# Performance work log

Measured on AMD Instinct MI355X. Metric: run time of the kernel, lower is better.

The kernel has to match this reference:

```python
import jax, jax.numpy as jnp
import numpy as np


def _log_g(x):
    # log_g(x) = log(relu(x)+1) if x >= 0 else x
    return jnp.where(x >= 0, jnp.log1p(jnp.maximum(x, 0.0)), x)


def _min_gru(hg):
    # hg: [B, H, L] -> [B, H/2, L]
    h, gate = jnp.split(hg, 2, axis=1)
    log_coeffs = -jax.nn.softplus(gate)                    # log(1 - z)
    log_values = -jax.nn.softplus(-gate) + _log_g(h)       # log(z) + log g(h)
    a_star = jnp.cumsum(log_coeffs, axis=2)
    log_h0_plus_b_star = jax.lax.cumlogsumexp(log_values - a_star, axis=2)
    return jnp.exp(a_star + log_h0_plus_b_star)


def setup_inputs() -> dict:
    key = jax.random.key(0)
    B, H, L = 8, 512, 8192
    x = jax.random.normal(key, (B, H, L), dtype=jnp.float32)
    return {"x": x}


def reference(x) -> jnp.ndarray:
    # bidirectional minGRU: forward scan on first half of channels,
    # reversed scan on second half.
    fore, back = jnp.split(x, 2, axis=1)
    out_fore = _min_gru(fore)
    out_back = jnp.flip(_min_gru(jnp.flip(back, axis=2)), axis=2)
    return jnp.concatenate([out_fore, out_back], axis=1)  # [B, H/2, L]
```

## Files before the change

### kernel.cpp

```cpp
#include <hip/hip_runtime.h>
#include <math.h>


#define SEQ_L 8192
#define PER_LANE 8
#define SUB (64 * PER_LANE)
#define NSUB (SEQ_L / SUB)
#define DQ 4

__global__ __launch_bounds__(64, 2) void mingru_scan_kernel(
    const float* __restrict__ x, float* __restrict__ out) {
    const int blk = blockIdx.x;
    const int dir = blk >> 10;
    const int s   = blk & 1023;
    const int b   = s >> 7;
    const int c   = s & 127;
    const int lane = threadIdx.x;

    const float* __restrict__ hrow = x + (size_t)((b * 512) + (dir * 256) + c) * SEQ_L;
    const float* __restrict__ grow = hrow + (size_t)128 * SEQ_L;
    float* __restrict__ orow = out + (size_t)((b * 256) + (dir * 128) + c) * SEQ_L;

    float4 qh0[DQ], qh1[DQ], qg0[DQ], qg1[DQ];

#pragma unroll
    for (int k = 0; k < DQ; ++k) {
        const int base = k * SUB + lane * PER_LANE;
        const int p = dir ? (SEQ_L - base - PER_LANE) : base;
        qh0[k] = *(const float4*)(hrow + p);
        qh1[k] = *(const float4*)(hrow + p + 4);
        qg0[k] = *(const float4*)(grow + p);
        qg1[k] = *(const float4*)(grow + p + 4);
    }

    float carry = 0.0f;

#pragma unroll
    for (int t = 0; t < NSUB; ++t) {
        const int slot = t & (DQ - 1);
        const float4 h0 = qh0[slot], h1 = qh1[slot];
        const float4 g0 = qg0[slot], g1 = qg1[slot];

        if (t + DQ < NSUB) {
            const int nb = (t + DQ) * SUB + lane * PER_LANE;
            const int np = dir ? (SEQ_L - nb - PER_LANE) : nb;
            qh0[slot] = *(const float4*)(hrow + np);
            qh1[slot] = *(const float4*)(hrow + np + 4);
            qg0[slot] = *(const float4*)(grow + np);
            qg1[slot] = *(const float4*)(grow + np + 4);
        }

        float hv[PER_LANE], gv[PER_LANE];
        if (dir == 0) {
            hv[0]=h0.x; hv[1]=h0.y; hv[2]=h0.z; hv[3]=h0.w;
            hv[4]=h1.x; hv[5]=h1.y; hv[6]=h1.z; hv[7]=h1.w;
            gv[0]=g0.x; gv[1]=g0.y; gv[2]=g0.z; gv[3]=g0.w;
            gv[4]=g1.x; gv[5]=g1.y; gv[6]=g1.z; gv[7]=g1.w;
        } else {
            hv[0]=h1.w; hv[1]=h1.z; hv[2]=h1.y; hv[3]=h1.x;
            hv[4]=h0.w; hv[5]=h0.z; hv[6]=h0.y; hv[7]=h0.x;
            gv[0]=g1.w; gv[1]=g1.z; gv[2]=g1.y; gv[3]=g1.x;
            gv[4]=g0.w; gv[5]=g0.z; gv[6]=g0.y; gv[7]=g0.x;
        }

        float pp[PER_LANE], ov0[PER_LANE];
        float ca = 1.0f, cb = 0.0f;
#pragma unroll
        for (int j = 0; j < PER_LANE; ++j) {
            const float gt = gv[j];
            const float e  = __expf(-fabsf(gt));
            const float r  = 1.0f / (1.0f + e);
            const float sn = e * r;
            const float z  = (gt >= 0.0f) ? r  : sn;
            const float a  = (gt >= 0.0f) ? sn : r;
            const float hh = hv[j];
            const float gf = (hh >= 0.0f) ? (hh + 1.0f) : __expf(hh);
            const float bb = z * gf;
            cb = a * cb + bb;
            ca = a * ca;
            ov0[j] = cb;
            pp[j]  = ca;
        }

        float pa = ca, pb = cb;
#pragma unroll
        for (int d = 1; d < 64; d <<= 1) {
            const float oa = __shfl_up(pa, d);
            const float ob = __shfl_up(pb, d);
            if (lane >= d) {
                pb = pa * ob + pb;
                pa = pa * oa;
            }
        }

        float ea = __shfl_up(pa, 1);
        float eb = __shfl_up(pb, 1);
        if (lane == 0) { ea = 1.0f; eb = 0.0f; }
        const float st = ea * carry + eb;

        float ov[PER_LANE];
#pragma unroll
        for (int j = 0; j < PER_LANE; ++j) ov[j] = ov0[j] + st * pp[j];

        const int base = t * SUB + lane * PER_LANE;
        if (dir == 0) {
            *(float4*)(orow + base)     = make_float4(ov[0], ov[1], ov[2], ov[3]);
            *(float4*)(orow + base + 4) = make_float4(ov[4], ov[5], ov[6], ov[7]);
        } else {
            const int p = SEQ_L - base - PER_LANE;
            *(float4*)(orow + p)     = make_float4(ov[7], ov[6], ov[5], ov[4]);
            *(float4*)(orow + p + 4) = make_float4(ov[3], ov[2], ov[1], ov[0]);
        }

        const float ga = __shfl(pa, 63);
        const float gb = __shfl(pb, 63);
        carry = ga * carry + gb;
    }
}

extern "C" void kernel_launch(void* const* d_in, const int* in_sizes, int n_in,
                              void* d_out, int out_size, void* d_ws, size_t ws_size,
                              hipStream_t stream) {
    const float* x = (const float*)d_in[0];
    float* out = (float*)d_out;
    mingru_scan_kernel<<<2048, 64, 0, stream>>>(x, out);
}
```

Before: 218.3 us.

## Split sequential scan into chunk-aggregate, state-propagate, and apply kernels

Replaces the one-wavefront-per-sequence serial scan with a three-pass chunked scan. Pass one computes each 512-element chunk's affine aggregate, pass two serially propagates the carry across the 16 chunks of each sequence, and pass three recomputes the local scan with the carried-in state and writes the output. The goal is to expose far more parallelism than the original 2048 wavefronts with a 16-step serial dependency. The cost is reading the input twice, recomputing the gate math twice, and two extra kernel launches plus workspace traffic.

```diff
diff --git a/kernel.cpp b/kernel.cpp
--- a/kernel.cpp
+++ b/kernel.cpp
@@ -4,117 +4,149 @@
 
 #define SEQ_L 8192
 #define PER_LANE 8
-#define SUB (64 * PER_LANE)
-#define NSUB (SEQ_L / SUB)
-#define DQ 4
+#define CHUNK 512
+#define NCHUNK (SEQ_L / CHUNK)
+#define NSEQ 2048
+#define NCHUNK_TOTAL (NSEQ * NCHUNK)
 
-__global__ __launch_bounds__(64, 2) void mingru_scan_kernel(
-    const float* __restrict__ x, float* __restrict__ out) {
-    const int blk = blockIdx.x;
-    const int dir = blk >> 10;
-    const int s   = blk & 1023;
-    const int b   = s >> 7;
-    const int c   = s & 127;
-    const int lane = threadIdx.x;
+__device__ __forceinline__ void chunk_addr(const float* __restrict__ x,
+                                           int gchunk, int lane,
+                                           const float*& hrow, const float*& grow,
+                                           int& seq, int& k, int& dir, int& p) {
+    seq = gchunk >> 4;
+    k   = gchunk & 15;
+    dir = seq >> 10;
+    const int s = seq & 1023;
+    const int b = s >> 7;
+    const int c = s & 127;
+    hrow = x + (size_t)((b * 512) + (dir * 256) + c) * SEQ_L;
+    grow = hrow + (size_t)128 * SEQ_L;
+    const int base = k * CHUNK + lane * PER_LANE;
+    p = dir ? (SEQ_L - base - PER_LANE) : base;
+}
 
-    const float* __restrict__ hrow = x + (size_t)((b * 512) + (dir * 256) + c) * SEQ_L;
-    const float* __restrict__ grow = hrow + (size_t)128 * SEQ_L;
+__device__ __forceinline__ void load8(const float* hrow, const float* grow,
+                                      int p, int dir,
+                                      float* hv, float* gv) {
+    const float4 h0 = *(const float4*)(hrow + p);
+    const float4 h1 = *(const float4*)(hrow + p + 4);
+    const float4 g0 = *(const float4*)(grow + p);
+    const float4 g1 = *(const float4*)(grow + p + 4);
+    if (dir == 0) {
+        hv[0]=h0.x; hv[1]=h0.y; hv[2]=h0.z; hv[3]=h0.w;
+        hv[4]=h1.x; hv[5]=h1.y; hv[6]=h1.z; hv[7]=h1.w;
+        gv[0]=g0.x; gv[1]=g0.y; gv[2]=g0.z; gv[3]=g0.w;
+        gv[4]=g1.x; gv[5]=g1.y; gv[6]=g1.z; gv[7]=g1.w;
+    } else {
+        hv[0]=h1.w; hv[1]=h1.z; hv[2]=h1.y; hv[3]=h1.x;
+        hv[4]=h0.w; hv[5]=h0.z; hv[6]=h0.y; hv[7]=h0.x;
+        gv[0]=g1.w; gv[1]=g1.z; gv[2]=g1.y; gv[3]=g1.x;
+        gv[4]=g0.w; gv[5]=g0.z; gv[6]=g0.y; gv[7]=g0.x;
+    }
+}
+
+__device__ __forceinline__ void coeffs(float gt, float hh, float& a, float& bb) {
+    const float e  = __expf(-fabsf(gt));
+    const float r  = 1.0f / (1.0f + e);
+    const float sn = e * r;
+    const float z  = (gt >= 0.0f) ? r  : sn;
+    a  = (gt >= 0.0f) ? sn : r;
+    const float gf = (hh >= 0.0f) ? (hh + 1.0f) : __expf(hh);
+    bb = z * gf;
+}
+
+__global__ __launch_bounds__(256) void k_agg(const float* __restrict__ x,
+                                             float2* __restrict__ agg) {
+    const int lane = threadIdx.x & 63;
+    const int gchunk = blockIdx.x * 4 + (threadIdx.x >> 6);
+    const float *hrow, *grow; int seq, k, dir, p;
+    chunk_addr(x, gchunk, lane, hrow, grow, seq, k, dir, p);
+
+    float hv[PER_LANE], gv[PER_LANE];
+    load8(hrow, grow, p, dir, hv, gv);
+
+    float pa = 1.0f, pb = 0.0f;
+#pragma unroll
+    for (int j = 0; j < PER_LANE; ++j) {
+        float a, bb; coeffs(gv[j], hv[j], a, bb);
+        pb = a * pb + bb;
+        pa = a * pa;
+    }
+#pragma unroll
+    for (int d = 1; d < 64; d <<= 1) {
+        const float oa = __shfl_down(pa, d);
+        const float ob = __shfl_down(pb, d);
+        pa = pa * oa;
+        pb = oa * pb + ob;
+    }
+    if (lane == 0) agg[gchunk] = make_float2(pa, pb);
+}
+
+__global__ __launch_bounds__(256) void k_states(const float2* __restrict__ agg,
+                                                float* __restrict__ st) {
+    const int seq = blockIdx.x * 256 + threadIdx.x;
+    float s = 0.0f;
+#pragma unroll
+    for (int k = 0; k < NCHUNK; ++k) {
+        st[seq * NCHUNK + k] = s;
+        const float2 ab = agg[seq * NCHUNK + k];
+        s = ab.x * s + ab.y;
+    }
+}
+
+__global__ __launch_bounds__(256) void k_apply(const float* __restrict__ x,
+                                               const float* __restrict__ st,
+                                               float* __restrict__ out) {
+    const int lane = threadIdx.x & 63;
+    const int gchunk = blockIdx.x * 4 + (threadIdx.x >> 6);
+    const float *hrow, *grow; int seq, k, dir, p;
+    chunk_addr(x, gchunk, lane, hrow, grow, seq, k, dir, p);
+
+    const int s_  = seq & 1023;
+    const int b   = s_ >> 7;
+    const int c   = s_ & 127;
     float* __restrict__ orow = out + (size_t)((b * 256) + (dir * 128) + c) * SEQ_L;
 
-    float4 qh0[DQ], qh1[DQ], qg0[DQ], qg1[DQ];
+    float hv[PER_LANE], gv[PER_LANE];
+    load8(hrow, grow, p, dir, hv, gv);
+    const float chunk_state = st[gchunk];
 
+    float pp[PER_LANE], ov0[PER_LANE];
+    float ca = 1.0f, cb = 0.0f;
 #pragma unroll
-    for (int k = 0; k < DQ; ++k) {
-        const int base = k * SUB + lane * PER_LANE;
-        const int p = dir ? (SEQ_L - base - PER_LANE) : base;
-        qh0[k] = *(const float4*)(hrow + p);
-        qh1[k] = *(const float4*)(hrow + p + 4);
-        qg0[k] = *(const float4*)(grow + p);
-        qg1[k] = *(const float4*)(grow + p + 4);
+    for (int j = 0; j < PER_LANE; ++j) {
+        float a, bb; coeffs(gv[j], hv[j], a, bb);
+        cb = a * cb + bb;
+        ca = a * ca;
+        ov0[j] = cb;
+        pp[j]  = ca;
     }
 
-    float carry = 0.0f;
+    float pa = ca, pb = cb;
+#pragma unroll
+    for (int d = 1; d < 64; d <<= 1) {
+        const float oa = __shfl_up(pa, d);
+        const float ob = __shfl_up(pb, d);
+        if (lane >= d) {
+            pb = pa * ob + pb;
+            pa = pa * oa;
+        }
+    }
+    float ea = __shfl_up(pa, 1);
+    float eb = __shfl_up(pb, 1);
+    if (lane == 0) { ea = 1.0f; eb = 0.0f; }
+    const float stl = ea * chunk_state + eb;
 
+    float ov[PER_LANE];
 #pragma unroll
-    for (int t = 0; t < NSUB; ++t) {
-        const int slot = t & (DQ - 1);
-        const float4 h0 = qh0[slot], h1 = qh1[slot];
-        const float4 g0 = qg0[slot], g1 = qg1[slot];
+    for (int j = 0; j < PER_LANE; ++j) ov[j] = ov0[j] + stl * pp[j];
 
-        if (t + DQ < NSUB) {
-            const int nb = (t + DQ) * SUB + lane * PER_LANE;
-            const int np = dir ? (SEQ_L - nb - PER_LANE) : nb;
-            qh0[slot] = *(const float4*)(hrow + np);
-            qh1[slot] = *(const float4*)(hrow + np + 4);
-            qg0[slot] = *(const float4*)(grow + np);
-            qg1[slot] = *(const float4*)(grow + np + 4);
-        }
-
-        float hv[PER_LANE], gv[PER_LANE];
-        if (dir == 0) {
-            hv[0]=h0.x; hv[1]=h0.y; hv[2]=h0.z; hv[3]=h0.w;
-            hv[4]=h1.x; hv[5]=h1.y; hv[6]=h1.z; hv[7]=h1.w;
-            gv[0]=g0.x; gv[1]=g0.y; gv[2]=g0.z; gv[3]=g0.w;
-            gv[4]=g1.x; gv[5]=g1.y; gv[6]=g1.z; gv[7]=g1.w;
-        } else {
-            hv[0]=h1.w; hv[1]=h1.z; hv[2]=h1.y; hv[3]=h1.x;
-            hv[4]=h0.w; hv[5]=h0.z; hv[6]=h0.y; hv[7]=h0.x;
-            gv[0]=g1.w; gv[1]=g1.z; gv[2]=g1.y; gv[3]=g1.x;
-            gv[4]=g0.w; gv[5]=g0.z; gv[6]=g0.y; gv[7]=g0.x;
-        }
-
-        float pp[PER_LANE], ov0[PER_LANE];
-        float ca = 1.0f, cb = 0.0f;
-#pragma unroll
-        for (int j = 0; j < PER_LANE; ++j) {
-            const float gt = gv[j];
-            const float e  = __expf(-fabsf(gt));
-            const float r  = 1.0f / (1.0f + e);
-            const float sn = e * r;
-            const float z  = (gt >= 0.0f) ? r  : sn;
-            const float a  = (gt >= 0.0f) ? sn : r;
-            const float hh = hv[j];
-            const float gf = (hh >= 0.0f) ? (hh + 1.0f) : __expf(hh);
-            const float bb = z * gf;
-            cb = a * cb + bb;
-            ca = a * ca;
-            ov0[j] = cb;
-            pp[j]  = ca;
-        }
-
-        float pa = ca, pb = cb;
-#pragma unroll
-        for (int d = 1; d < 64; d <<= 1) {
-            const float oa = __shfl_up(pa, d);
-            const float ob = __shfl_up(pb, d);
-            if (lane >= d) {
-                pb = pa * ob + pb;
-                pa = pa * oa;
-            }
-        }
-
-        float ea = __shfl_up(pa, 1);
-        float eb = __shfl_up(pb, 1);
-        if (lane == 0) { ea = 1.0f; eb = 0.0f; }
-        const float st = ea * carry + eb;
-
-        float ov[PER_LANE];
-#pragma unroll
-        for (int j = 0; j < PER_LANE; ++j) ov[j] = ov0[j] + st * pp[j];
-
-        const int base = t * SUB + lane * PER_LANE;
-        if (dir == 0) {
-            *(float4*)(orow + base)     = make_float4(ov[0], ov[1], ov[2], ov[3]);
-            *(float4*)(orow + base + 4) = make_float4(ov[4], ov[5], ov[6], ov[7]);
-        } else {
-            const int p = SEQ_L - base - PER_LANE;
-            *(float4*)(orow + p)     = make_float4(ov[7], ov[6], ov[5], ov[4]);
-            *(float4*)(orow + p + 4) = make_float4(ov[3], ov[2], ov[1], ov[0]);
-        }
-
-        const float ga = __shfl(pa, 63);
-        const float gb = __shfl(pb, 63);
-        carry = ga * carry + gb;
+    if (dir == 0) {
+        *(float4*)(orow + p)     = make_float4(ov[0], ov[1], ov[2], ov[3]);
+        *(float4*)(orow + p + 4) = make_float4(ov[4], ov[5], ov[6], ov[7]);
+    } else {
+        *(float4*)(orow + p)     = make_float4(ov[7], ov[6], ov[5], ov[4]);
+        *(float4*)(orow + p + 4) = make_float4(ov[3], ov[2], ov[1], ov[0]);
     }
 }
 
@@ -123,5 +155,10 @@
                               hipStream_t stream) {
     const float* x = (const float*)d_in[0];
     float* out = (float*)d_out;
-    mingru_scan_kernel<<<2048, 64, 0, stream>>>(x, out);
+    float2* agg = (float2*)d_ws;
+    float* st   = (float*)((char*)d_ws + NCHUNK_TOTAL * sizeof(float2));
+
+    k_agg   <<<NCHUNK_TOTAL / 4, 256, 0, stream>>>(x, agg);
+    k_states<<<NSEQ / 256,       256, 0, stream>>>(agg, st);
+    k_apply <<<NCHUNK_TOTAL / 4, 256, 0, stream>>>(x, st, out);
 }
```

New measurement: 227.9 us. +4.4%, slower.
